# Performance work log

Hardware: AMD Instinct MI355X
Metric: run time of the kernel (lower is better)

The kernel has to match this reference:

```python
import jax, jax.numpy as jnp
import numpy as np

B, K, N, D, L = 16, 16, 1024, 256, 8
LN_EPS = 1e-5


def setup_inputs() -> dict:
    key = jax.random.key(0)
    ks = jax.random.split(key, 12)
    w = lambda k, sh: jax.random.normal(k, sh, jnp.float32) * 0.02
    return {
        "H": jax.random.normal(ks[0], (B, K, N, D), jnp.float32),
        "eps": jax.random.normal(ks[1], (B, L, D), jnp.float32),  # single Gaussian draw per batch
        "mu": jnp.zeros((1, L, D), jnp.float32),
        "log_sigma": jnp.full((1, L, D), -2.0, jnp.float32),
        "Wq": w(ks[2], (D, D)), "bq": jnp.zeros((D,), jnp.float32),
        "Wk": w(ks[3], (D, D)), "bk": jnp.zeros((D,), jnp.float32),
        "Wv": w(ks[4], (D, D)), "bv": jnp.zeros((D,), jnp.float32),
        "W_ih": w(ks[5], (3 * D, D)), "b_ih": jnp.zeros((3 * D,), jnp.float32),
        "W_hh": w(ks[6], (3 * D, D)), "b_hh": jnp.zeros((3 * D,), jnp.float32),
        "W1": w(ks[7], (D, D)), "b1": jnp.zeros((D,), jnp.float32),
        "W2": w(ks[8], (D, D)), "b2": jnp.zeros((D,), jnp.float32),
        "ln_g": jnp.ones((D,), jnp.float32), "ln_b": jnp.zeros((D,), jnp.float32),
    }


def reference(H, eps, mu, log_sigma, Wq, bq, Wk, bk, Wv, bv,
              W_ih, b_ih, W_hh, b_hh, W1, b1, W2, b2, ln_g, ln_b):
    d = H.shape[-1]
    scale = 1.0 / jnp.sqrt(jnp.asarray(d, H.dtype))
    slots0 = mu + jnp.exp(log_sigma) * eps  # [B,L,D]

    def step(slots, h_t):  # slots [B,L,D], h_t [B,N,D]
        Q = slots @ Wq.T + bq
        Kt = h_t @ Wk.T + bk
        V = h_t @ Wv.T + bv
        scores = jnp.einsum("bld,bnd->bln", Q, Kt) * scale
        attn = jnp.nan_to_num(jax.nn.softmax(scores, axis=-1))
        upd = jnp.einsum("bln,bnd->bld", attn, V)
        # torch.nn.GRUCell(input=upd, hidden=slots)
        gi = upd @ W_ih.T + b_ih
        gh = slots @ W_hh.T + b_hh
        ir, iz, inn = jnp.split(gi, 3, axis=-1)
        hr, hz, hn = jnp.split(gh, 3, axis=-1)
        r = jax.nn.sigmoid(ir + hr)
        z = jax.nn.sigmoid(iz + hz)
        n = jnp.tanh(inn + r * hn)
        s2 = (1.0 - z) * n + z * slots
        # FFN + residual + LayerNorm
        ffn = jnp.maximum(s2 @ W1.T + b1, 0.0) @ W2.T + b2
        x = s2 + ffn
        mean = x.mean(axis=-1, keepdims=True)
        var = x.var(axis=-1, keepdims=True)
        s3 = (x - mean) / jnp.sqrt(var + LN_EPS) * ln_g + ln_b
        return s3, (s3, attn)

    _, (S, Beta) = jax.lax.scan(step, slots0, jnp.swapaxes(H, 0, 1))
    return jnp.swapaxes(S, 0, 1), jnp.swapaxes(Beta, 0, 1)  # [B,K,L,D], [B,K,L,N]
```

## Files before the change

kernel.cpp:

```cpp
#include <hip/hip_runtime.h>
#include <math.h>


#define Bn 16
#define KK 16
#define Nn 1024
#define Dn 256
#define Ln 8

#define OFF_WQK   0
#define OFF_BQK   65536
#define OFF_WGIT  65792
#define OFF_BGI   262400
#define OFF_WHHT  263168
#define OFF_W1T   459776
#define OFF_W2T   525312
#define OFF_SLOTS 590848
#define OFF_QK    623616
#define OFF_PAV   656384
#define OFF_PDEN  1704960
#define OFF_PG    1709056
#define OFF_PX    4854784
#define OFF_DENS  4920320
#define OFF_S2G   4922368

__device__ __forceinline__ float sigmoidf_(float x) { return 1.f / (1.f + __expf(-x)); }

__global__ __launch_bounds__(256) void p1_kernel(
    const float* __restrict__ Wq, const float* __restrict__ bq,
    const float* __restrict__ Wk, float* __restrict__ Wqk, float* __restrict__ bqk) {
  int w = blockIdx.x, tid = threadIdx.x;
  if (w < 256) {
    float acc = 0.f;
#pragma unroll 8
    for (int a = 0; a < 256; ++a) acc += Wq[a * 256 + w] * Wk[a * 256 + tid];
    Wqk[w * 256 + tid] = acc;
  } else {
    float acc = 0.f;
#pragma unroll 8
    for (int a = 0; a < 256; ++a) acc += bq[a] * Wk[a * 256 + tid];
    bqk[tid] = acc;
  }
}

__global__ __launch_bounds__(256) void p2_kernel(
    const float* __restrict__ Wih, const float* __restrict__ bih,
    const float* __restrict__ Wv, const float* __restrict__ bv,
    float* __restrict__ WgiT, float* __restrict__ bgi) {
  int d = blockIdx.x, tid = threadIdx.x;
  float a0 = 0.f, a1 = 0.f, a2 = 0.f;
#pragma unroll 4
  for (int c = 0; c < 256; ++c) {
    float wv = Wv[c * 256 + d];
    a0 += Wih[tid * 256 + c] * wv;
    a1 += Wih[(tid + 256) * 256 + c] * wv;
    a2 += Wih[(tid + 512) * 256 + c] * wv;
  }
  WgiT[d * 768 + tid] = a0;
  WgiT[d * 768 + 256 + tid] = a1;
  WgiT[d * 768 + 512 + tid] = a2;
  if (d < 3) {
    int jj = d * 256 + tid;
    float s = bih[jj];
    for (int c = 0; c < 256; ++c) s += Wih[jj * 256 + c] * bv[c];
    bgi[jj] = s;
  }
}

__global__ __launch_bounds__(256) void p3_kernel(
    const float* __restrict__ Whh, const float* __restrict__ W1,
    const float* __restrict__ W2, float* __restrict__ WhhT,
    float* __restrict__ W1T, float* __restrict__ W2T) {
  __shared__ float tile[32][33];
  int wg = blockIdx.x, tid = threadIdx.x;
  const float* in; float* out; int R, C, tr, tc;
  if (wg < 192)      { in = Whh; out = WhhT; R = 768; C = 256; wg -= 0;   tr = wg >> 3; tc = wg & 7; }
  else if (wg < 256) { in = W1;  out = W1T;  R = 256; C = 256; wg -= 192; tr = wg >> 3; tc = wg & 7; }
  else               { in = W2;  out = W2T;  R = 256; C = 256; wg -= 256; tr = wg >> 3; tc = wg & 7; }
  int r = tid >> 5, c = tid & 31;
#pragma unroll
  for (int k = 0; k < 4; ++k)
    tile[r + 8 * k][c] = in[(tr * 32 + r + 8 * k) * C + tc * 32 + c];
  __syncthreads();
#pragma unroll
  for (int k = 0; k < 4; ++k)
    out[(tc * 32 + r + 8 * k) * R + tr * 32 + c] = tile[c][r + 8 * k];
}

__global__ __launch_bounds__(256) void init_slots_kernel(
    const float* __restrict__ eps, const float* __restrict__ mu,
    const float* __restrict__ lsig, float* __restrict__ slots) {
  int idx = blockIdx.x * 256 + threadIdx.x;
  int r = idx & 2047;
  slots[idx] = mu[r] + expf(lsig[r]) * eps[idx];
}

__global__ __launch_bounds__(256) void qk0_kernel(
    const float* __restrict__ Wqk, const float* __restrict__ bqk,
    const float* __restrict__ slots, float* __restrict__ Qkout) {
  __shared__ float sl_s[2048];
  int j = blockIdx.x & 7, b = blockIdx.x >> 3, tid = threadIdx.x;
  for (int k = 0; k < 8; ++k) sl_s[tid + k * 256] = slots[b * 2048 + tid + k * 256];
  __syncthreads();
  int l = tid >> 5, ee = j * 32 + (tid & 31);
  float acc = bqk[ee];
#pragma unroll 8
  for (int d = 0; d < 256; ++d) acc += sl_s[l * 256 + d] * Wqk[d * 256 + ee];
  Qkout[b * 2048 + l * 256 + ee] = acc;
}

__global__ __launch_bounds__(256) void attn_kernel(
    const float* __restrict__ H, const float* __restrict__ Qk,
    float* __restrict__ beta_out, float* __restrict__ par_av,
    float* __restrict__ par_den, int t) {
  __shared__ float h_s[32 * 258];
  __shared__ float qk_s[Ln * Dn];
  __shared__ float e_s[256];
  __shared__ float red[256];
  int tile = blockIdx.x, b = blockIdx.y, tid = threadIdx.x;
#pragma unroll
  for (int k = 0; k < 8; ++k) qk_s[tid + k * 256] = Qk[b * 2048 + tid + k * 256];
  const float* Hbase = H + (((long)b * KK + t) * Nn + tile * 32) * Dn;
  const float4* src = (const float4*)Hbase;
#pragma unroll
  for (int k = 0; k < 8; ++k) {
    int idx4 = tid + k * 256;
    int r = idx4 >> 6, d4 = idx4 & 63;
    float4 v = src[idx4];
    float* dst = &h_s[r * 258 + d4 * 4];
    ((float2*)dst)[0] = make_float2(v.x, v.y);
    ((float2*)dst)[1] = make_float2(v.z, v.w);
  }
  __syncthreads();
  int l = tid >> 5, row = tid & 31;
  {
    const float2* hr2 = (const float2*)(&h_s[row * 258]);
    const float2* qr2 = (const float2*)(&qk_s[l * 256]);
    float acc = 0.f;
#pragma unroll 8
    for (int e = 0; e < 128; ++e) {
      float2 hv = hr2[e], qv = qr2[e];
      acc += hv.x * qv.x + hv.y * qv.y;
    }
    float ev = __expf(acc * 0.0625f);
    e_s[tid] = ev;
    red[tid] = ev;
    beta_out[(((long)b * KK + t) * Ln + l) * Nn + tile * 32 + row] = ev;
  }
  __syncthreads();
  if (tid < 8) {
    float s = 0.f;
    for (int i = 0; i < 32; ++i) s += red[tid * 32 + i];
    par_den[(b * 32 + tile) * 8 + tid] = s;
  }
  float av[8];
#pragma unroll
  for (int i = 0; i < 8; ++i) av[i] = 0.f;
  for (int rr = 0; rr < 32; ++rr) {
    float hv = h_s[rr * 258 + tid];
#pragma unroll
    for (int i = 0; i < 8; ++i) av[i] += e_s[i * 32 + rr] * hv;
  }
  long pbase = (long)(b * 32 + tile) * 2048;
#pragma unroll
  for (int i = 0; i < 8; ++i) par_av[pbase + i * 256 + tid] = av[i];
}

__global__ __launch_bounds__(1024) void gru_kernel(
    const float* __restrict__ WgiT, const float* __restrict__ WhhT,
    const float* __restrict__ par_av, const float* __restrict__ par_den,
    const float* __restrict__ slots, float* __restrict__ pg,
    float* __restrict__ dens_all, int t) {
  __shared__ float w_s[16 * 768];
  __shared__ float rupd[8][128];
  __shared__ float upd_s[128];
  __shared__ float sl_s[128];
  __shared__ float den_s[8];
  int b = blockIdx.x & 15, kc = blockIdx.x >> 4;
  int tid = threadIdx.x;

  const float4* wsrc = (const float4*)(WgiT + kc * 12288);
  float4 wv0 = wsrc[tid], wv1 = wsrc[tid + 1024], wv2 = wsrc[tid + 2048];
  {
    int g = tid >> 7, le = tid & 127;
    int l = le >> 4, e = le & 15;
    float ps = 0.f;
    long base = ((long)(b * 32)) * 2048 + l * 256 + kc * 16 + e;
#pragma unroll
    for (int i = 0; i < 4; ++i) ps += par_av[base + (long)(g * 4 + i) * 2048];
    rupd[g][le] = ps;
  }
  if (tid < 256) {
    int ll = tid >> 5, tl = tid & 31;
    float dv = par_den[(b * 32 + tl) * 8 + ll];
#pragma unroll
    for (int m = 1; m < 32; m <<= 1) dv += __shfl_xor(dv, m);
    if (tl == 0) den_s[ll] = 1.f / dv;
  }
  if (tid < 128) sl_s[tid] = slots[b * 2048 + (tid >> 4) * 256 + kc * 16 + (tid & 15)];
  ((float4*)w_s)[tid] = wv0;
  ((float4*)w_s)[tid + 1024] = wv1;
  ((float4*)w_s)[tid + 2048] = wv2;
  __syncthreads();

  if (kc == 0 && tid < 8) dens_all[(t * 16 + b) * 8 + tid] = den_s[tid];
  if (tid < 128) {
    float s = 0.f;
#pragma unroll
    for (int g = 0; g < 8; ++g) s += rupd[g][tid];
    upd_s[tid] = s * den_s[tid >> 4];
  }
  __syncthreads();

  int l4 = tid >> 8, cb = tid & 255;
  long pb0 = ((long)(b * 16 + kc) * 8 + l4) * 1536;
  long pb1 = ((long)(b * 16 + kc) * 8 + l4 + 4) * 1536;
  {
    float a0 = 0.f, a1 = 0.f, a2 = 0.f, a3 = 0.f, a4 = 0.f, a5 = 0.f;
#pragma unroll
    for (int e = 0; e < 16; ++e) {
      float u0 = upd_s[l4 * 16 + e];
      float u1 = upd_s[(l4 + 4) * 16 + e];
      float w0 = w_s[e * 768 + cb];
      float w1 = w_s[e * 768 + 256 + cb];
      float w2 = w_s[e * 768 + 512 + cb];
      a0 += u0 * w0; a1 += u0 * w1; a2 += u0 * w2;
      a3 += u1 * w0; a4 += u1 * w1; a5 += u1 * w2;
    }
    pg[pb0 + cb] = a0; pg[pb0 + 256 + cb] = a1; pg[pb0 + 512 + cb] = a2;
    pg[pb1 + cb] = a3; pg[pb1 + 256 + cb] = a4; pg[pb1 + 512 + cb] = a5;
  }
  __syncthreads();
  {
    const float4* hsrc = (const float4*)(WhhT + kc * 12288);
    ((float4*)w_s)[tid] = hsrc[tid];
    ((float4*)w_s)[tid + 1024] = hsrc[tid + 1024];
    ((float4*)w_s)[tid + 2048] = hsrc[tid + 2048];
  }
  __syncthreads();
  {
    float a0 = 0.f, a1 = 0.f, a2 = 0.f, a3 = 0.f, a4 = 0.f, a5 = 0.f;
#pragma unroll
    for (int e = 0; e < 16; ++e) {
      float s0 = sl_s[l4 * 16 + e];
      float s1 = sl_s[(l4 + 4) * 16 + e];
      float w0 = w_s[e * 768 + cb];
      float w1 = w_s[e * 768 + 256 + cb];
      float w2 = w_s[e * 768 + 512 + cb];
      a0 += s0 * w0; a1 += s0 * w1; a2 += s0 * w2;
      a3 += s1 * w0; a4 += s1 * w1; a5 += s1 * w2;
    }
    pg[pb0 + 768 + cb] = a0; pg[pb0 + 1024 + cb] = a1; pg[pb0 + 1280 + cb] = a2;
    pg[pb1 + 768 + cb] = a3; pg[pb1 + 1024 + cb] = a4; pg[pb1 + 1280 + cb] = a5;
  }
}

__global__ __launch_bounds__(1024) void chain2a_kernel(
    const float* __restrict__ pg, const float* __restrict__ bgi,
    const float* __restrict__ bhh,
    const float* __restrict__ W1T, const float* __restrict__ b1,
    const float* __restrict__ W2T,
    const float* __restrict__ slots, float* __restrict__ s2g,
    float* __restrict__ px) {
  __shared__ float gsum[1536];
  __shared__ float s2_s[256];
  __shared__ float f1s[128];
  __shared__ float red8[128 * 9];
  __shared__ float red4[1024];
  int wid = blockIdx.x;
  int b = wid & 15, l = (wid >> 4) & 7, ph = wid >> 7;
  int tid = threadIdx.x;

  for (int col = tid; col < 1536; col += 1024) {
    float v[16];
#pragma unroll
    for (int j = 0; j < 16; ++j) v[j] = pg[((long)(b * 16 + j) * 8 + l) * 1536 + col];
    float a = 0.f;
#pragma unroll
    for (int j = 0; j < 16; ++j) a += v[j];
    gsum[col] = a;
  }
  __syncthreads();
  if (tid < 256) {
    int c = tid;
    float r = sigmoidf_(gsum[c] + bgi[c] + gsum[768 + c] + bhh[c]);
    float z = sigmoidf_(gsum[256 + c] + bgi[256 + c] + gsum[1024 + c] + bhh[256 + c]);
    float n = tanhf(gsum[512 + c] + bgi[512 + c] + r * (gsum[1280 + c] + bhh[512 + c]));
    float s2 = (1.f - z) * n + z * slots[b * 2048 + l * 256 + c];
    s2_s[c] = s2;
    if (ph == 0) s2g[b * 2048 + l * 256 + c] = s2;
  }
  __syncthreads();
  {
    int kc = tid >> 7, h = tid & 127;
    const float* wp = W1T + (kc * 32) * 256 + ph * 128 + h;
    const float* sp = s2_s + kc * 32;
    float acc = 0.f;
#pragma unroll
    for (int g = 0; g < 2; ++g) {
      float w[16];
#pragma unroll
      for (int i = 0; i < 16; ++i) w[i] = wp[(g * 16 + i) * 256];
#pragma unroll
      for (int i = 0; i < 16; ++i) acc += sp[g * 16 + i] * w[i];
    }
    red8[h * 9 + kc] = acc;
  }
  __syncthreads();
  if (tid < 128) {
    float a = b1[ph * 128 + tid];
#pragma unroll
    for (int kc = 0; kc < 8; ++kc) a += red8[tid * 9 + kc];
    f1s[tid] = fmaxf(a, 0.f);
  }
  __syncthreads();
  {
    int q = tid >> 8, c = tid & 255;
    const float* wp = W2T + (ph * 128 + q * 32) * 256 + c;
    const float* fp = f1s + q * 32;
    float acc = 0.f;
#pragma unroll
    for (int g = 0; g < 2; ++g) {
      float w[16];
#pragma unroll
      for (int i = 0; i < 16; ++i) w[i] = wp[(g * 16 + i) * 256];
#pragma unroll
      for (int i = 0; i < 16; ++i) acc += fp[g * 16 + i] * w[i];
    }
    red4[q * 256 + c] = acc;
  }
  __syncthreads();
  if (tid < 256)
    px[((long)(b * 8 + l) * 2 + ph) * 256 + tid] =
        red4[tid] + red4[256 + tid] + red4[512 + tid] + red4[768 + tid];
}

__global__ __launch_bounds__(1024) void chain2b_kernel(
    const float* __restrict__ px, const float* __restrict__ b2,
    const float* __restrict__ ln_g, const float* __restrict__ ln_b,
    const float* __restrict__ Wqk, const float* __restrict__ bqk,
    const float* __restrict__ s2g, float* __restrict__ slots,
    float* __restrict__ S, float* __restrict__ QkG, int t) {
  __shared__ float s3_s[256];
  __shared__ float red8[128 * 9];
  __shared__ float lnr[8];
  int wid = blockIdx.x;
  int b = wid & 15, l = (wid >> 4) & 7, ph = wid >> 7;
  int tid = threadIdx.x;
  if (tid < 256) {
    long pb = (long)(b * 8 + l) * 2 * 256;
    float x = px[pb + tid] + px[pb + 256 + tid] + b2[tid] + s2g[b * 2048 + l * 256 + tid];
    s3_s[tid] = x;
    float sr = x, qr = x * x;
#pragma unroll
    for (int m = 1; m < 64; m <<= 1) { sr += __shfl_xor(sr, m); qr += __shfl_xor(qr, m); }
    if ((tid & 63) == 0) { lnr[tid >> 6] = sr; lnr[4 + (tid >> 6)] = qr; }
  }
  __syncthreads();
  if (tid < 256) {
    float m = (lnr[0] + lnr[1] + lnr[2] + lnr[3]) * (1.f / 256.f);
    float v = (lnr[4] + lnr[5] + lnr[6] + lnr[7]) * (1.f / 256.f) - m * m;
    float s3 = (s3_s[tid] - m) * rsqrtf(v + 1e-5f) * ln_g[tid] + ln_b[tid];
    s3_s[tid] = s3;
    if (ph == 0) {
      S[(((long)(b * 16) + t) * 8 + l) * 256 + tid] = s3;
      slots[b * 2048 + l * 256 + tid] = s3;
    }
  }
  __syncthreads();
  {
    int kc = tid >> 7, c = tid & 127;
    const float* wp = Wqk + (kc * 32) * 256 + ph * 128 + c;
    const float* sp = s3_s + kc * 32;
    float acc = 0.f;
#pragma unroll
    for (int g = 0; g < 2; ++g) {
      float w[16];
#pragma unroll
      for (int i = 0; i < 16; ++i) w[i] = wp[(g * 16 + i) * 256];
#pragma unroll
      for (int i = 0; i < 16; ++i) acc += sp[g * 16 + i] * w[i];
    }
    red8[c * 9 + kc] = acc;
  }
  __syncthreads();
  if (tid < 128) {
    float a = bqk[ph * 128 + tid];
#pragma unroll
    for (int kc = 0; kc < 8; ++kc) a += red8[tid * 9 + kc];
    QkG[b * 2048 + l * 256 + ph * 128 + tid] = a;
  }
}

__global__ __launch_bounds__(1024) void beta_norm_kernel(
    const float* __restrict__ dens_all, float* __restrict__ Beta) {
  int wid = blockIdx.x;
  int b = wid >> 4, t = wid & 15;
  int tid = threadIdx.x;
  long base = (((long)b * 16) + t) * 8192;
#pragma unroll
  for (int i = 0; i < 8; ++i) {
    int idx = i * 1024 + tid;
    int l = idx >> 10;
    Beta[base + idx] *= dens_all[(t * 16 + b) * 8 + l];
  }
}

extern "C" void kernel_launch(void* const* d_in, const int* in_sizes, int n_in,
                              void* d_out, int out_size, void* d_ws, size_t ws_size,
                              hipStream_t stream) {
  const float* H    = (const float*)d_in[0];
  const float* eps  = (const float*)d_in[1];
  const float* mu   = (const float*)d_in[2];
  const float* lsig = (const float*)d_in[3];
  const float* Wq   = (const float*)d_in[4];
  const float* bq   = (const float*)d_in[5];
  const float* Wk   = (const float*)d_in[6];
  const float* Wv   = (const float*)d_in[8];
  const float* bv   = (const float*)d_in[9];
  const float* Wih  = (const float*)d_in[10];
  const float* bih  = (const float*)d_in[11];
  const float* Whh  = (const float*)d_in[12];
  const float* bhh  = (const float*)d_in[13];
  const float* W1   = (const float*)d_in[14];
  const float* b1   = (const float*)d_in[15];
  const float* W2   = (const float*)d_in[16];
  const float* b2   = (const float*)d_in[17];
  const float* ln_g = (const float*)d_in[18];
  const float* ln_b = (const float*)d_in[19];

  float* out = (float*)d_out;
  float* S    = out;
  float* Beta = out + (long)Bn * KK * Ln * Dn;

  float* ws = (float*)d_ws;
  float* Wqk   = ws + OFF_WQK;
  float* bqk   = ws + OFF_BQK;
  float* WgiT  = ws + OFF_WGIT;
  float* bgi   = ws + OFF_BGI;
  float* WhhT  = ws + OFF_WHHT;
  float* W1T   = ws + OFF_W1T;
  float* W2T   = ws + OFF_W2T;
  float* slots = ws + OFF_SLOTS;
  float* Qk    = ws + OFF_QK;
  float* pav   = ws + OFF_PAV;
  float* pden  = ws + OFF_PDEN;
  float* pg    = ws + OFF_PG;
  float* px    = ws + OFF_PX;
  float* dens  = ws + OFF_DENS;
  float* s2g   = ws + OFF_S2G;

  p1_kernel<<<257, 256, 0, stream>>>(Wq, bq, Wk, Wqk, bqk);
  p2_kernel<<<256, 256, 0, stream>>>(Wih, bih, Wv, bv, WgiT, bgi);
  p3_kernel<<<320, 256, 0, stream>>>(Whh, W1, W2, WhhT, W1T, W2T);
  init_slots_kernel<<<128, 256, 0, stream>>>(eps, mu, lsig, slots);
  qk0_kernel<<<128, 256, 0, stream>>>(Wqk, bqk, slots, Qk);

  for (int t = 0; t < KK; ++t) {
    attn_kernel<<<dim3(32, 16), 256, 0, stream>>>(H, Qk, Beta, pav, pden, t);
    gru_kernel<<<256, 1024, 0, stream>>>(WgiT, WhhT, pav, pden, slots, pg, dens, t);
    chain2a_kernel<<<256, 1024, 0, stream>>>(pg, bgi, bhh, W1T, b1, W2T, slots, s2g, px);
    chain2b_kernel<<<256, 1024, 0, stream>>>(px, b2, ln_g, ln_b, Wqk, bqk,
                                             s2g, slots, S, Qk, t);
  }
  beta_norm_kernel<<<256, 1024, 0, stream>>>(dens, Beta);
}
```

Baseline: 932.5 us.

## Fuse GRU-tail, FFN and LayerNorm kernels, merge prologue, retile attention scores

Merges the two per-step chain kernels into one, so each block recomputes the full FFN for its (b,l) row redundantly across the two ph halves. Slots are double-buffered to remove the write-after-read hazard this creates. The four setup kernels become one prologue launch. The attention score dot product is retiled so each thread holds two H rows in registers and computes partial sums over an e-slice, reduced through shared memory. The goal is to cut per-step launches and the intermediate px/s2g global traffic, at the cost of duplicated FFN work and more shared memory in the attention kernel.

Result: faster. 888.4 us (-4.7%).

```diff
diff --git a/kernel.cpp b/kernel.cpp
--- a/kernel.cpp
+++ b/kernel.cpp
@@ -16,83 +16,80 @@
 #define OFF_W1T   459776
 #define OFF_W2T   525312
 #define OFF_SLOTS 590848
-#define OFF_QK    623616
-#define OFF_PAV   656384
-#define OFF_PDEN  1704960
-#define OFF_PG    1709056
-#define OFF_PX    4854784
-#define OFF_DENS  4920320
-#define OFF_S2G   4922368
+#define OFF_QK    656384
+#define OFF_PAV   689152
+#define OFF_PDEN  1737728
+#define OFF_PG    1741824
+#define OFF_DENS  4887552
 
 __device__ __forceinline__ float sigmoidf_(float x) { return 1.f / (1.f + __expf(-x)); }
 
-__global__ __launch_bounds__(256) void p1_kernel(
+__global__ __launch_bounds__(256) void prologue_kernel(
     const float* __restrict__ Wq, const float* __restrict__ bq,
-    const float* __restrict__ Wk, float* __restrict__ Wqk, float* __restrict__ bqk) {
-  int w = blockIdx.x, tid = threadIdx.x;
-  if (w < 256) {
-    float acc = 0.f;
-#pragma unroll 8
-    for (int a = 0; a < 256; ++a) acc += Wq[a * 256 + w] * Wk[a * 256 + tid];
-    Wqk[w * 256 + tid] = acc;
-  } else {
-    float acc = 0.f;
-#pragma unroll 8
-    for (int a = 0; a < 256; ++a) acc += bq[a] * Wk[a * 256 + tid];
-    bqk[tid] = acc;
-  }
-}
-
-__global__ __launch_bounds__(256) void p2_kernel(
+    const float* __restrict__ Wk,
     const float* __restrict__ Wih, const float* __restrict__ bih,
     const float* __restrict__ Wv, const float* __restrict__ bv,
-    float* __restrict__ WgiT, float* __restrict__ bgi) {
-  int d = blockIdx.x, tid = threadIdx.x;
-  float a0 = 0.f, a1 = 0.f, a2 = 0.f;
-#pragma unroll 4
-  for (int c = 0; c < 256; ++c) {
-    float wv = Wv[c * 256 + d];
-    a0 += Wih[tid * 256 + c] * wv;
-    a1 += Wih[(tid + 256) * 256 + c] * wv;
-    a2 += Wih[(tid + 512) * 256 + c] * wv;
-  }
-  WgiT[d * 768 + tid] = a0;
-  WgiT[d * 768 + 256 + tid] = a1;
-  WgiT[d * 768 + 512 + tid] = a2;
-  if (d < 3) {
-    int jj = d * 256 + tid;
-    float s = bih[jj];
-    for (int c = 0; c < 256; ++c) s += Wih[jj * 256 + c] * bv[c];
-    bgi[jj] = s;
-  }
-}
-
-__global__ __launch_bounds__(256) void p3_kernel(
     const float* __restrict__ Whh, const float* __restrict__ W1,
-    const float* __restrict__ W2, float* __restrict__ WhhT,
-    float* __restrict__ W1T, float* __restrict__ W2T) {
+    const float* __restrict__ W2,
+    const float* __restrict__ eps, const float* __restrict__ mu,
+    const float* __restrict__ lsig,
+    float* __restrict__ Wqk, float* __restrict__ bqk,
+    float* __restrict__ WgiT, float* __restrict__ bgi,
+    float* __restrict__ WhhT, float* __restrict__ W1T, float* __restrict__ W2T,
+    float* __restrict__ slots) {
   __shared__ float tile[32][33];
   int wg = blockIdx.x, tid = threadIdx.x;
-  const float* in; float* out; int R, C, tr, tc;
-  if (wg < 192)      { in = Whh; out = WhhT; R = 768; C = 256; wg -= 0;   tr = wg >> 3; tc = wg & 7; }
-  else if (wg < 256) { in = W1;  out = W1T;  R = 256; C = 256; wg -= 192; tr = wg >> 3; tc = wg & 7; }
-  else               { in = W2;  out = W2T;  R = 256; C = 256; wg -= 256; tr = wg >> 3; tc = wg & 7; }
-  int r = tid >> 5, c = tid & 31;
-#pragma unroll
-  for (int k = 0; k < 4; ++k)
-    tile[r + 8 * k][c] = in[(tr * 32 + r + 8 * k) * C + tc * 32 + c];
-  __syncthreads();
-#pragma unroll
-  for (int k = 0; k < 4; ++k)
-    out[(tc * 32 + r + 8 * k) * R + tr * 32 + c] = tile[c][r + 8 * k];
-}
-
-__global__ __launch_bounds__(256) void init_slots_kernel(
-    const float* __restrict__ eps, const float* __restrict__ mu,
-    const float* __restrict__ lsig, float* __restrict__ slots) {
-  int idx = blockIdx.x * 256 + threadIdx.x;
-  int r = idx & 2047;
-  slots[idx] = mu[r] + expf(lsig[r]) * eps[idx];
+  if (wg < 257) {
+    int w = wg;
+    if (w < 256) {
+      float acc = 0.f;
+#pragma unroll 8
+      for (int a = 0; a < 256; ++a) acc += Wq[a * 256 + w] * Wk[a * 256 + tid];
+      Wqk[w * 256 + tid] = acc;
+    } else {
+      float acc = 0.f;
+#pragma unroll 8
+      for (int a = 0; a < 256; ++a) acc += bq[a] * Wk[a * 256 + tid];
+      bqk[tid] = acc;
+    }
+  } else if (wg < 513) {
+    int d = wg - 257;
+    float a0 = 0.f, a1 = 0.f, a2 = 0.f;
+#pragma unroll 4
+    for (int c = 0; c < 256; ++c) {
+      float wv = Wv[c * 256 + d];
+      a0 += Wih[tid * 256 + c] * wv;
+      a1 += Wih[(tid + 256) * 256 + c] * wv;
+      a2 += Wih[(tid + 512) * 256 + c] * wv;
+    }
+    WgiT[d * 768 + tid] = a0;
+    WgiT[d * 768 + 256 + tid] = a1;
+    WgiT[d * 768 + 512 + tid] = a2;
+    if (d < 3) {
+      int jj = d * 256 + tid;
+      float s = bih[jj];
+      for (int c = 0; c < 256; ++c) s += Wih[jj * 256 + c] * bv[c];
+      bgi[jj] = s;
+    }
+  } else if (wg < 833) {
+    int sub = wg - 513;
+    const float* in; float* out; int R, C, tr, tc;
+    if (sub < 192)      { in = Whh; out = WhhT; R = 768; C = 256; tr = sub >> 3; tc = sub & 7; }
+    else if (sub < 256) { in = W1;  out = W1T;  R = 256; C = 256; sub -= 192; tr = sub >> 3; tc = sub & 7; }
+    else                { in = W2;  out = W2T;  R = 256; C = 256; sub -= 256; tr = sub >> 3; tc = sub & 7; }
+    int r = tid >> 5, c = tid & 31;
+#pragma unroll
+    for (int k = 0; k < 4; ++k)
+      tile[r + 8 * k][c] = in[(tr * 32 + r + 8 * k) * C + tc * 32 + c];
+    __syncthreads();
+#pragma unroll
+    for (int k = 0; k < 4; ++k)
+      out[(tc * 32 + r + 8 * k) * R + tr * 32 + c] = tile[c][r + 8 * k];
+  } else {
+    int idx = (wg - 833) * 256 + tid;
+    int r = idx & 2047;
+    slots[idx] = mu[r] + expf(lsig[r]) * eps[idx];
+  }
 }
 
 __global__ __launch_bounds__(256) void qk0_kernel(
@@ -113,37 +110,56 @@
     const float* __restrict__ H, const float* __restrict__ Qk,
     float* __restrict__ beta_out, float* __restrict__ par_av,
     float* __restrict__ par_den, int t) {
-  __shared__ float h_s[32 * 258];
-  __shared__ float qk_s[Ln * Dn];
-  __shared__ float e_s[256];
+  __shared__ float h_s[32 * 260];
+  __shared__ float qk_s[8 * 260];
+  __shared__ float red_a[8 * 256];
+  __shared__ float es2[32 * 8];
   __shared__ float red[256];
   int tile = blockIdx.x, b = blockIdx.y, tid = threadIdx.x;
 #pragma unroll
-  for (int k = 0; k < 8; ++k) qk_s[tid + k * 256] = Qk[b * 2048 + tid + k * 256];
-  const float* Hbase = H + (((long)b * KK + t) * Nn + tile * 32) * Dn;
-  const float4* src = (const float4*)Hbase;
-#pragma unroll
   for (int k = 0; k < 8; ++k) {
-    int idx4 = tid + k * 256;
-    int r = idx4 >> 6, d4 = idx4 & 63;
-    float4 v = src[idx4];
-    float* dst = &h_s[r * 258 + d4 * 4];
-    ((float2*)dst)[0] = make_float2(v.x, v.y);
-    ((float2*)dst)[1] = make_float2(v.z, v.w);
-  }
-  __syncthreads();
-  int l = tid >> 5, row = tid & 31;
-  {
-    const float2* hr2 = (const float2*)(&h_s[row * 258]);
-    const float2* qr2 = (const float2*)(&qk_s[l * 256]);
-    float acc = 0.f;
-#pragma unroll 8
-    for (int e = 0; e < 128; ++e) {
-      float2 hv = hr2[e], qv = qr2[e];
-      acc += hv.x * qv.x + hv.y * qv.y;
-    }
-    float ev = __expf(acc * 0.0625f);
-    e_s[tid] = ev;
+    int idx = tid + k * 256, l = idx >> 8, e = idx & 255;
+    qk_s[l * 260 + e] = Qk[b * 2048 + idx];
+  }
+  const float4* src = (const float4*)(H + (((long)b * KK + t) * Nn + tile * 32) * Dn);
+#pragma unroll
+  for (int k = 0; k < 8; ++k) {
+    int idx4 = tid + k * 256, r = idx4 >> 6, d4 = idx4 & 63;
+    *(float4*)(&h_s[r * 260 + d4 * 4]) = src[idx4];
+  }
+  __syncthreads();
+  {
+    int eg = tid >> 5, lh = (tid >> 4) & 1, rq = tid & 15;
+    float4 hA[8], hB[8];
+    const float4* ha = (const float4*)(&h_s[(rq * 2) * 260 + eg * 32]);
+    const float4* hb = (const float4*)(&h_s[(rq * 2 + 1) * 260 + eg * 32]);
+#pragma unroll
+    for (int i = 0; i < 8; ++i) { hA[i] = ha[i]; hB[i] = hb[i]; }
+    float acc[4][2] = {{0.f, 0.f}, {0.f, 0.f}, {0.f, 0.f}, {0.f, 0.f}};
+#pragma unroll
+    for (int li = 0; li < 4; ++li) {
+      const float4* qv = (const float4*)(&qk_s[(lh * 4 + li) * 260 + eg * 32]);
+#pragma unroll
+      for (int i = 0; i < 8; ++i) {
+        float4 qq = qv[i];
+        acc[li][0] += qq.x * hA[i].x + qq.y * hA[i].y + qq.z * hA[i].z + qq.w * hA[i].w;
+        acc[li][1] += qq.x * hB[i].x + qq.y * hB[i].y + qq.z * hB[i].z + qq.w * hB[i].w;
+      }
+    }
+#pragma unroll
+    for (int li = 0; li < 4; ++li) {
+      red_a[eg * 256 + (lh * 4 + li) * 32 + rq * 2] = acc[li][0];
+      red_a[eg * 256 + (lh * 4 + li) * 32 + rq * 2 + 1] = acc[li][1];
+    }
+  }
+  __syncthreads();
+  {
+    int l = tid >> 5, row = tid & 31;
+    float a = 0.f;
+#pragma unroll
+    for (int eg = 0; eg < 8; ++eg) a += red_a[eg * 256 + l * 32 + row];
+    float ev = __expf(a * 0.0625f);
+    es2[row * 8 + l] = ev;
     red[tid] = ev;
     beta_out[(((long)b * KK + t) * Ln + l) * Nn + tile * 32 + row] = ev;
   }
@@ -153,13 +169,13 @@
     for (int i = 0; i < 32; ++i) s += red[tid * 32 + i];
     par_den[(b * 32 + tile) * 8 + tid] = s;
   }
-  float av[8];
-#pragma unroll
-  for (int i = 0; i < 8; ++i) av[i] = 0.f;
+  float av[8] = {0.f, 0.f, 0.f, 0.f, 0.f, 0.f, 0.f, 0.f};
   for (int rr = 0; rr < 32; ++rr) {
-    float hv = h_s[rr * 258 + tid];
-#pragma unroll
-    for (int i = 0; i < 8; ++i) av[i] += e_s[i * 32 + rr] * hv;
+    float hv = h_s[rr * 260 + tid];
+    float4 ea = *(const float4*)(&es2[rr * 8]);
+    float4 eb = *(const float4*)(&es2[rr * 8 + 4]);
+    av[0] += ea.x * hv; av[1] += ea.y * hv; av[2] += ea.z * hv; av[3] += ea.w * hv;
+    av[4] += eb.x * hv; av[5] += eb.y * hv; av[6] += eb.z * hv; av[7] += eb.w * hv;
   }
   long pbase = (long)(b * 32 + tile) * 2048;
 #pragma unroll
@@ -169,7 +185,7 @@
 __global__ __launch_bounds__(1024) void gru_kernel(
     const float* __restrict__ WgiT, const float* __restrict__ WhhT,
     const float* __restrict__ par_av, const float* __restrict__ par_den,
-    const float* __restrict__ slots, float* __restrict__ pg,
+    const float* __restrict__ slots_cur, float* __restrict__ pg,
     float* __restrict__ dens_all, int t) {
   __shared__ float w_s[16 * 768];
   __shared__ float rupd[8][128];
@@ -197,7 +213,7 @@
     for (int m = 1; m < 32; m <<= 1) dv += __shfl_xor(dv, m);
     if (tl == 0) den_s[ll] = 1.f / dv;
   }
-  if (tid < 128) sl_s[tid] = slots[b * 2048 + (tid >> 4) * 256 + kc * 16 + (tid & 15)];
+  if (tid < 128) sl_s[tid] = slots_cur[b * 2048 + (tid >> 4) * 256 + kc * 16 + (tid & 15)];
   ((float4*)w_s)[tid] = wv0;
   ((float4*)w_s)[tid + 1024] = wv1;
   ((float4*)w_s)[tid + 2048] = wv2;
@@ -255,122 +271,97 @@
   }
 }
 
-__global__ __launch_bounds__(1024) void chain2a_kernel(
+__global__ __launch_bounds__(1024) void chainm_kernel(
     const float* __restrict__ pg, const float* __restrict__ bgi,
     const float* __restrict__ bhh,
     const float* __restrict__ W1T, const float* __restrict__ b1,
-    const float* __restrict__ W2T,
-    const float* __restrict__ slots, float* __restrict__ s2g,
-    float* __restrict__ px) {
+    const float* __restrict__ W2T, const float* __restrict__ b2,
+    const float* __restrict__ Wqk, const float* __restrict__ bqk,
+    const float* __restrict__ ln_g, const float* __restrict__ ln_b,
+    const float* __restrict__ slots_cur, float* __restrict__ slots_nxt,
+    float* __restrict__ S, float* __restrict__ QkG, int t) {
   __shared__ float gsum[1536];
-  __shared__ float s2_s[256];
-  __shared__ float f1s[128];
-  __shared__ float red8[128 * 9];
+  __shared__ float s2_s[256], f1s[256], s3_s[256];
   __shared__ float red4[1024];
-  int wid = blockIdx.x;
-  int b = wid & 15, l = (wid >> 4) & 7, ph = wid >> 7;
-  int tid = threadIdx.x;
-
-  for (int col = tid; col < 1536; col += 1024) {
-    float v[16];
-#pragma unroll
-    for (int j = 0; j < 16; ++j) v[j] = pg[((long)(b * 16 + j) * 8 + l) * 1536 + col];
-    float a = 0.f;
-#pragma unroll
-    for (int j = 0; j < 16; ++j) a += v[j];
-    gsum[col] = a;
-  }
-  __syncthreads();
-  if (tid < 256) {
-    int c = tid;
-    float r = sigmoidf_(gsum[c] + bgi[c] + gsum[768 + c] + bhh[c]);
-    float z = sigmoidf_(gsum[256 + c] + bgi[256 + c] + gsum[1024 + c] + bhh[256 + c]);
-    float n = tanhf(gsum[512 + c] + bgi[512 + c] + r * (gsum[1280 + c] + bhh[512 + c]));
-    float s2 = (1.f - z) * n + z * slots[b * 2048 + l * 256 + c];
-    s2_s[c] = s2;
-    if (ph == 0) s2g[b * 2048 + l * 256 + c] = s2;
-  }
-  __syncthreads();
-  {
-    int kc = tid >> 7, h = tid & 127;
-    const float* wp = W1T + (kc * 32) * 256 + ph * 128 + h;
-    const float* sp = s2_s + kc * 32;
-    float acc = 0.f;
-#pragma unroll
-    for (int g = 0; g < 2; ++g) {
-      float w[16];
-#pragma unroll
-      for (int i = 0; i < 16; ++i) w[i] = wp[(g * 16 + i) * 256];
-#pragma unroll
-      for (int i = 0; i < 16; ++i) acc += sp[g * 16 + i] * w[i];
-    }
-    red8[h * 9 + kc] = acc;
-  }
-  __syncthreads();
-  if (tid < 128) {
-    float a = b1[ph * 128 + tid];
-#pragma unroll
-    for (int kc = 0; kc < 8; ++kc) a += red8[tid * 9 + kc];
-    f1s[tid] = fmaxf(a, 0.f);
-  }
-  __syncthreads();
-  {
-    int q = tid >> 8, c = tid & 255;
-    const float* wp = W2T + (ph * 128 + q * 32) * 256 + c;
-    const float* fp = f1s + q * 32;
-    float acc = 0.f;
-#pragma unroll
-    for (int g = 0; g < 2; ++g) {
-      float w[16];
-#pragma unroll
-      for (int i = 0; i < 16; ++i) w[i] = wp[(g * 16 + i) * 256];
-#pragma unroll
-      for (int i = 0; i < 16; ++i) acc += fp[g * 16 + i] * w[i];
-    }
-    red4[q * 256 + c] = acc;
-  }
-  __syncthreads();
-  if (tid < 256)
-    px[((long)(b * 8 + l) * 2 + ph) * 256 + tid] =
-        red4[tid] + red4[256 + tid] + red4[512 + tid] + red4[768 + tid];
-}
-
-__global__ __launch_bounds__(1024) void chain2b_kernel(
-    const float* __restrict__ px, const float* __restrict__ b2,
-    const float* __restrict__ ln_g, const float* __restrict__ ln_b,
-    const float* __restrict__ Wqk, const float* __restrict__ bqk,
-    const float* __restrict__ s2g, float* __restrict__ slots,
-    float* __restrict__ S, float* __restrict__ QkG, int t) {
-  __shared__ float s3_s[256];
   __shared__ float red8[128 * 9];
   __shared__ float lnr[8];
   int wid = blockIdx.x;
   int b = wid & 15, l = (wid >> 4) & 7, ph = wid >> 7;
-  int tid = threadIdx.x;
+  int tid = threadIdx.x, q = tid >> 8, c = tid & 255;
+
+  for (int col = tid; col < 1536; col += 1024) {
+    float v[16];
+#pragma unroll
+    for (int j = 0; j < 16; ++j) v[j] = pg[((long)(b * 16 + j) * 8 + l) * 1536 + col];
+    float a = 0.f;
+#pragma unroll
+    for (int j = 0; j < 16; ++j) a += v[j];
+    gsum[col] = a;
+  }
+  __syncthreads();
   if (tid < 256) {
-    long pb = (long)(b * 8 + l) * 2 * 256;
-    float x = px[pb + tid] + px[pb + 256 + tid] + b2[tid] + s2g[b * 2048 + l * 256 + tid];
-    s3_s[tid] = x;
+    float r = sigmoidf_(gsum[c] + bgi[c] + gsum[768 + c] + bhh[c]);
+    float z = sigmoidf_(gsum[256 + c] + bgi[256 + c] + gsum[1024 + c] + bhh[256 + c]);
+    float n = tanhf(gsum[512 + c] + bgi[512 + c] + r * (gsum[1280 + c] + bhh[512 + c]));
+    s2_s[c] = (1.f - z) * n + z * slots_cur[b * 2048 + l * 256 + c];
+  }
+  __syncthreads();
+  {
+    const float* wp = W1T + (q * 64) * 256 + c;
+    const float* sp = s2_s + q * 64;
+    float acc = 0.f;
+#pragma unroll
+    for (int g = 0; g < 4; ++g) {
+      float w[16];
+#pragma unroll
+      for (int i = 0; i < 16; ++i) w[i] = wp[(g * 16 + i) * 256];
+#pragma unroll
+      for (int i = 0; i < 16; ++i) acc += sp[g * 16 + i] * w[i];
+    }
+    red4[q * 256 + c] = acc;
+  }
+  __syncthreads();
+  if (tid < 256)
+    f1s[c] = fmaxf(red4[c] + red4[256 + c] + red4[512 + c] + red4[768 + c] + b1[c], 0.f);
+  __syncthreads();
+  {
+    const float* wp = W2T + (q * 64) * 256 + c;
+    const float* fp = f1s + q * 64;
+    float acc = 0.f;
+#pragma unroll
+    for (int g = 0; g < 4; ++g) {
+      float w[16];
+#pragma unroll
+      for (int i = 0; i < 16; ++i) w[i] = wp[(g * 16 + i) * 256];
+#pragma unroll
+      for (int i = 0; i < 16; ++i) acc += fp[g * 16 + i] * w[i];
+    }
+    red4[q * 256 + c] = acc;
+  }
+  __syncthreads();
+  if (tid < 256) {
+    float x = red4[c] + red4[256 + c] + red4[512 + c] + red4[768 + c] + b2[c] + s2_s[c];
+    s3_s[c] = x;
     float sr = x, qr = x * x;
 #pragma unroll
     for (int m = 1; m < 64; m <<= 1) { sr += __shfl_xor(sr, m); qr += __shfl_xor(qr, m); }
-    if ((tid & 63) == 0) { lnr[tid >> 6] = sr; lnr[4 + (tid >> 6)] = qr; }
+    if ((c & 63) == 0) { lnr[c >> 6] = sr; lnr[4 + (c >> 6)] = qr; }
   }
   __syncthreads();
   if (tid < 256) {
     float m = (lnr[0] + lnr[1] + lnr[2] + lnr[3]) * (1.f / 256.f);
     float v = (lnr[4] + lnr[5] + lnr[6] + lnr[7]) * (1.f / 256.f) - m * m;
-    float s3 = (s3_s[tid] - m) * rsqrtf(v + 1e-5f) * ln_g[tid] + ln_b[tid];
-    s3_s[tid] = s3;
+    float s3 = (s3_s[c] - m) * rsqrtf(v + 1e-5f) * ln_g[c] + ln_b[c];
+    s3_s[c] = s3;
     if (ph == 0) {
-      S[(((long)(b * 16) + t) * 8 + l) * 256 + tid] = s3;
-      slots[b * 2048 + l * 256 + tid] = s3;
-    }
-  }
-  __syncthreads();
-  {
-    int kc = tid >> 7, c = tid & 127;
-    const float* wp = Wqk + (kc * 32) * 256 + ph * 128 + c;
+      S[(((long)(b * 16) + t) * 8 + l) * 256 + c] = s3;
+      slots_nxt[b * 2048 + l * 256 + c] = s3;
+    }
+  }
+  __syncthreads();
+  {
+    int kc = tid >> 7, cc = tid & 127;
+    const float* wp = Wqk + (kc * 32) * 256 + ph * 128 + cc;
     const float* sp = s3_s + kc * 32;
     float acc = 0.f;
 #pragma unroll
@@ -381,7 +372,7 @@
 #pragma unroll
       for (int i = 0; i < 16; ++i) acc += sp[g * 16 + i] * w[i];
     }
-    red8[c * 9 + kc] = acc;
+    red8[cc * 9 + kc] = acc;
   }
   __syncthreads();
   if (tid < 128) {
@@ -434,34 +425,33 @@
   float* Beta = out + (long)Bn * KK * Ln * Dn;
 
   float* ws = (float*)d_ws;
-  float* Wqk   = ws + OFF_WQK;
-  float* bqk   = ws + OFF_BQK;
-  float* WgiT  = ws + OFF_WGIT;
-  float* bgi   = ws + OFF_BGI;
-  float* WhhT  = ws + OFF_WHHT;
-  float* W1T   = ws + OFF_W1T;
-  float* W2T   = ws + OFF_W2T;
-  float* slots = ws + OFF_SLOTS;
-  float* Qk    = ws + OFF_QK;
-  float* pav   = ws + OFF_PAV;
-  float* pden  = ws + OFF_PDEN;
-  float* pg    = ws + OFF_PG;
-  float* px    = ws + OFF_PX;
-  float* dens  = ws + OFF_DENS;
-  float* s2g   = ws + OFF_S2G;
-
-  p1_kernel<<<257, 256, 0, stream>>>(Wq, bq, Wk, Wqk, bqk);
-  p2_kernel<<<256, 256, 0, stream>>>(Wih, bih, Wv, bv, WgiT, bgi);
-  p3_kernel<<<320, 256, 0, stream>>>(Whh, W1, W2, WhhT, W1T, W2T);
-  init_slots_kernel<<<128, 256, 0, stream>>>(eps, mu, lsig, slots);
-  qk0_kernel<<<128, 256, 0, stream>>>(Wqk, bqk, slots, Qk);
+  float* Wqk    = ws + OFF_WQK;
+  float* bqk    = ws + OFF_BQK;
+  float* WgiT   = ws + OFF_WGIT;
+  float* bgi    = ws + OFF_BGI;
+  float* WhhT   = ws + OFF_WHHT;
+  float* W1T    = ws + OFF_W1T;
+  float* W2T    = ws + OFF_W2T;
+  float* slots0 = ws + OFF_SLOTS;
+  float* Qk     = ws + OFF_QK;
+  float* pav    = ws + OFF_PAV;
+  float* pden   = ws + OFF_PDEN;
+  float* pg     = ws + OFF_PG;
+  float* dens   = ws + OFF_DENS;
+
+  prologue_kernel<<<961, 256, 0, stream>>>(Wq, bq, Wk, Wih, bih, Wv, bv, Whh, W1, W2,
+                                           eps, mu, lsig,
+                                           Wqk, bqk, WgiT, bgi, WhhT, W1T, W2T, slots0);
+  qk0_kernel<<<128, 256, 0, stream>>>(Wqk, bqk, slots0, Qk);
 
   for (int t = 0; t < KK; ++t) {
+    float* scur = slots0 + (t & 1) * 32768;
+    float* snxt = slots0 + ((t + 1) & 1) * 32768;
     attn_kernel<<<dim3(32, 16), 256, 0, stream>>>(H, Qk, Beta, pav, pden, t);
-    gru_kernel<<<256, 1024, 0, stream>>>(WgiT, WhhT, pav, pden, slots, pg, dens, t);
-    chain2a_kernel<<<256, 1024, 0, stream>>>(pg, bgi, bhh, W1T, b1, W2T, slots, s2g, px);
-    chain2b_kernel<<<256, 1024, 0, stream>>>(px, b2, ln_g, ln_b, Wqk, bqk,
-                                             s2g, slots, S, Qk, t);
+    gru_kernel<<<256, 1024, 0, stream>>>(WgiT, WhhT, pav, pden, scur, pg, dens, t);
+    chainm_kernel<<<256, 1024, 0, stream>>>(pg, bgi, bhh, W1T, b1, W2T, b2,
+                                            Wqk, bqk, ln_g, ln_b, scur, snxt,
+                                            S, Qk, t);
   }
   beta_norm_kernel<<<256, 1024, 0, stream>>>(dens, Beta);
 }
```
